# Optimization experiments

Hardware: AMD Instinct MI355X
Metric: run time of the kernel (lower is better)

The kernel has to match this reference:

```python
import jax, jax.numpy as jnp
import numpy as np

B, S, D, H = 2, 2048, 1024, 16
DK = D // H

def setup_inputs() -> dict:
    key = jax.random.key(0)
    ks = jax.random.split(key, 8)
    q = jax.random.normal(ks[0], (B, S, D), dtype=jnp.float32)
    k = jax.random.normal(ks[1], (B, S, D), dtype=jnp.float32)
    v = jax.random.normal(ks[2], (B, S, D), dtype=jnp.float32)
    # causal mask [B, S, S]; masked_fill where mask == 0
    mask = jnp.broadcast_to(jnp.tril(jnp.ones((S, S), dtype=jnp.int32)), (B, S, S))
    sc = 1.0 / np.sqrt(D)
    w_q = jax.random.normal(ks[3], (D, D), dtype=jnp.float32) * sc
    w_k = jax.random.normal(ks[4], (D, D), dtype=jnp.float32) * sc
    w_v = jax.random.normal(ks[5], (D, D), dtype=jnp.float32) * sc
    w_o = jax.random.normal(ks[6], (D, D), dtype=jnp.float32) * sc
    b_o = jnp.zeros((D,), dtype=jnp.float32)
    return {"query": q, "key": k, "value": v, "mask": mask,
            "w_q": w_q, "w_k": w_k, "w_v": w_v, "w_o": w_o, "b_o": b_o}

def reference(query, key, value, mask, w_q, w_k, w_v, w_o, b_o):
    # torch nn.Linear: y = x @ W.T
    def split_heads(x):
        return x.reshape(B, S, H, DK).transpose(0, 2, 1, 3)  # [B,H,S,DK]
    Q = split_heads(query @ w_q.T)
    K = split_heads(key @ w_k.T)
    V = split_heads(value @ w_v.T)
    scores = jnp.einsum('bhsd,bhtd->bhst', Q, K) / np.sqrt(DK)  # [B,H,S,S]
    m = mask[:, None, :, :]  # broadcast over heads
    scores = jnp.where(m == 0, jnp.float32(-1e9), scores)
    attn = jax.nn.softmax(scores, axis=-1)
    # dropout is identity in eval mode
    out = jnp.einsum('bhst,bhtd->bhsd', attn, V)  # [B,H,S,DK]
    out = out.transpose(0, 2, 1, 3).reshape(B, S, D)
    out = out @ w_o.T + b_o
    return (out, attn)
```

## Files before the change

kernel.cpp:

```cpp
#include <hip/hip_runtime.h>
#include <hip/hip_bf16.h>

#define S_LEN 2048
#define DMODEL 1024
#define NHEAD 16
#define DKH 64
#define NBATCH 2
#define NBH (NBATCH * NHEAD)
#define MROWS (NBATCH * S_LEN)
#define C1 0.18033688011112042f
#define C2 28.853900817779268f

typedef short bf16x8 __attribute__((ext_vector_type(8)));
typedef float f32x16 __attribute__((ext_vector_type(16)));
typedef float f32x4 __attribute__((ext_vector_type(4)));

typedef __attribute__((address_space(3))) void lds_void;
typedef __attribute__((address_space(1))) const void gbl_void;

__device__ __forceinline__ ushort f2bf(float f) {
  __hip_bfloat16 h = __float2bfloat16(f);
  union { __hip_bfloat16 h; ushort u; } c; c.h = h; return c.u;
}

__device__ __forceinline__ uint pack2(float a, float b) {
  float2 t; t.x = a; t.y = b;
  __hip_bfloat162 h = __float22bfloat162_rn(t);
  union { __hip_bfloat162 h; uint u; } c; c.h = h; return c.u;
}

__device__ __forceinline__ float bf2f(ushort u) {
  union { float f; uint u; } c; c.u = ((uint)u) << 16; return c.f;
}

__device__ __forceinline__ void gld16(void* lds, const void* g) {
  __builtin_amdgcn_global_load_lds((gbl_void*)(uintptr_t)g,
                                   (lds_void*)(uintptr_t)lds, 16, 0, 0);
}

__device__ __forceinline__ void gload_tile128(char* lds, const ushort* src, int strideE,
                                              int wid, int lane) {
#pragma unroll
  for (int j = 0; j < 4; j++) {
    int r = wid * 32 + j * 8 + (lane >> 3);
    int c = lane & 7;
    const char* g = (const char*)(src + (size_t)r * strideE) + ((c ^ (r & 7)) << 4);
    gld16(lds + wid * 4096 + j * 1024, g);
  }
}

__device__ __forceinline__ bf16x8 lds_frag(const char* base, int row, int kbyte) {
  int byte = row * 128 + kbyte;
  byte ^= (row & 7) << 4;
  return *(const bf16x8*)(base + byte);
}

__device__ __forceinline__ void tile_load_regs(const ushort* src, int srcStride,
                                               int tid, uint4& a, uint4& b) {
  int r = tid >> 2, cb = (tid & 3) * 32;
  const char* s = (const char*)(src + (size_t)r * srcStride) + cb;
  a = *(const uint4*)s;
  b = *(const uint4*)(s + 16);
}

__device__ __forceinline__ void tile_write_lds(char* dst, int tid,
                                               const uint4& a, const uint4& b) {
  int r = tid >> 2, cb = (tid & 3) * 32;
  int base = r * 128 + cb;
  int sw = (r & 7) << 4;
  *(uint4*)(dst + (base ^ sw)) = a;
  *(uint4*)(dst + ((base + 16) ^ sw)) = b;
}

__global__ __launch_bounds__(256) void cvt_kernel(
    const float* __restrict__ s0, ushort* __restrict__ d0,
    const float* __restrict__ s1, ushort* __restrict__ d1,
    const float* __restrict__ s2, ushort* __restrict__ d2,
    const float* __restrict__ s3, ushort* __restrict__ d3,
    const float* __restrict__ s4, ushort* __restrict__ d4,
    const float* __restrict__ s5, ushort* __restrict__ d5,
    const float* __restrict__ s6, ushort* __restrict__ d6) {
  const float* src; ushort* dst; int n;
  switch (blockIdx.y) {
    case 0: src = s0; dst = d0; n = MROWS * DMODEL; break;
    case 1: src = s1; dst = d1; n = MROWS * DMODEL; break;
    case 2: src = s2; dst = d2; n = MROWS * DMODEL; break;
    case 3: src = s3; dst = d3; n = DMODEL * DMODEL; break;
    case 4: src = s4; dst = d4; n = DMODEL * DMODEL; break;
    case 5: src = s5; dst = d5; n = DMODEL * DMODEL; break;
    default: src = s6; dst = d6; n = DMODEL * DMODEL; break;
  }
  for (size_t i = ((size_t)blockIdx.x * 256 + threadIdx.x) * 8; i < (size_t)n;
       i += (size_t)gridDim.x * 256 * 8) {
    float4 a = *(const float4*)(src + i);
    float4 b = *(const float4*)(src + i + 4);
    uint4 o = { pack2(a.x, a.y), pack2(a.z, a.w), pack2(b.x, b.y), pack2(b.z, b.w) };
    *(uint4*)(dst + i) = o;
  }
}

__global__ __launch_bounds__(256) void proj_kernel(
    const ushort* __restrict__ Xq, const ushort* __restrict__ Wq, ushort* __restrict__ Oq,
    const ushort* __restrict__ Xk, const ushort* __restrict__ Wk, ushort* __restrict__ Ok,
    const ushort* __restrict__ Xv, const ushort* __restrict__ Wv, ushort* __restrict__ Ov) {
  __shared__ char smem[34816];
  char* Xt = smem;
  char* Wt = smem + 16384;
  const ushort* X; const ushort* W; ushort* outH;
  if (blockIdx.z == 0)      { X = Xq; W = Wq; outH = Oq; }
  else if (blockIdx.z == 1) { X = Xk; W = Wk; outH = Ok; }
  else                      { X = Xv; W = Wv; outH = Ov; }

  int bm = blockIdx.x, bn = blockIdx.y;
  int tid = threadIdx.x;
  int lane = tid & 63, wid = tid >> 6;
  int l31 = lane & 31, hi = lane >> 5;
  int wr = wid >> 1, wc = wid & 1;
  f32x16 acc[2][2] = {};

  for (int kt = 0; kt < 1024; kt += 64) {
    __syncthreads();
    gload_tile128(Xt, X + (size_t)bm * 128 * 1024 + kt, 1024, wid, lane);
    gload_tile128(Wt, W + (size_t)bn * 128 * 1024 + kt, 1024, wid, lane);
    __syncthreads();
#pragma unroll
    for (int kk = 0; kk < 4; kk++) {
      bf16x8 a0 = lds_frag(Xt, 64 * wr + l31,      kk * 32 + hi * 16);
      bf16x8 a1 = lds_frag(Xt, 64 * wr + 32 + l31, kk * 32 + hi * 16);
      bf16x8 b0 = lds_frag(Wt, 64 * wc + l31,      kk * 32 + hi * 16);
      bf16x8 b1 = lds_frag(Wt, 64 * wc + 32 + l31, kk * 32 + hi * 16);
      acc[0][0] = __builtin_amdgcn_mfma_f32_32x32x16_bf16(a0, b0, acc[0][0], 0, 0, 0);
      acc[0][1] = __builtin_amdgcn_mfma_f32_32x32x16_bf16(a0, b1, acc[0][1], 0, 0, 0);
      acc[1][0] = __builtin_amdgcn_mfma_f32_32x32x16_bf16(a1, b0, acc[1][0], 0, 0, 0);
      acc[1][1] = __builtin_amdgcn_mfma_f32_32x32x16_bf16(a1, b1, acc[1][1], 0, 0, 0);
    }
  }
  __syncthreads();
  if (blockIdx.z != 2) {
    ushort (*ot)[136] = (ushort (*)[136])smem;
#pragma unroll
    for (int mi = 0; mi < 2; mi++)
#pragma unroll
      for (int ni = 0; ni < 2; ni++) {
        int col = wc * 64 + ni * 32 + l31;
#pragma unroll
        for (int rr = 0; rr < 16; rr++) {
          int row = wr * 64 + mi * 32 + (rr & 3) + 8 * (rr >> 2) + 4 * hi;
          ot[row][col] = f2bf(acc[mi][ni][rr]);
        }
      }
    __syncthreads();
    int r2 = tid >> 1, half = tid & 1;
    int m = bm * 128 + r2, b = m >> 11, s = m & 2047;
    int h = bn * 2 + half;
    ushort* dst = outH + ((size_t)(b * NHEAD + h) * S_LEN + s) * DKH;
    const ushort* srow = &ot[r2][half * 64];
#pragma unroll
    for (int j = 0; j < 8; j++)
      *(uint4*)(dst + j * 8) = *(const uint4*)(srow + j * 8);
  } else {
    ushort (*otT)[136] = (ushort (*)[136])smem;
#pragma unroll
    for (int mi = 0; mi < 2; mi++)
#pragma unroll
      for (int ni = 0; ni < 2; ni++) {
        int col = wc * 64 + ni * 32 + l31;
#pragma unroll
        for (int rr = 0; rr < 16; rr++) {
          int row = wr * 64 + mi * 32 + (rr & 3) + 8 * (rr >> 2) + 4 * hi;
          otT[col][row] = f2bf(acc[mi][ni][rr]);
        }
      }
    __syncthreads();
    int col2 = tid >> 1, sh = (tid & 1) * 64;
    int b = bm >> 4, s0 = (bm & 15) * 128;
    int h = bn * 2 + (col2 >> 6), d = col2 & 63;
    ushort* dst = outH + ((size_t)(b * NHEAD + h) * DKH + d) * S_LEN + s0 + sh;
    const ushort* srow = &otT[col2][sh];
#pragma unroll
    for (int j = 0; j < 8; j++)
      *(uint4*)(dst + j * 8) = *(const uint4*)(srow + j * 8);
  }
}

__global__ __launch_bounds__(256) void outproj_kernel(const ushort* __restrict__ A,
                                                      const ushort* __restrict__ W,
                                                      const float* __restrict__ bias,
                                                      float* __restrict__ out) {
  __shared__ char smem[33792];
  char* Xt = smem;
  char* Wt = smem + 16384;
  int bm = blockIdx.x, bn = blockIdx.y;
  int tid = threadIdx.x;
  int lane = tid & 63, wid = tid >> 6;
  int l31 = lane & 31, hi = lane >> 5;
  int wr = wid >> 1, wc = wid & 1;
  f32x16 acc[2][2] = {};

  for (int kt = 0; kt < 1024; kt += 64) {
    __syncthreads();
    gload_tile128(Xt, A + (size_t)bm * 128 * 1024 + kt, 1024, wid, lane);
    gload_tile128(Wt, W + (size_t)bn * 128 * 1024 + kt, 1024, wid, lane);
    __syncthreads();
#pragma unroll
    for (int kk = 0; kk < 4; kk++) {
      bf16x8 a0 = lds_frag(Xt, 64 * wr + l31,      kk * 32 + hi * 16);
      bf16x8 a1 = lds_frag(Xt, 64 * wr + 32 + l31, kk * 32 + hi * 16);
      bf16x8 b0 = lds_frag(Wt, 64 * wc + l31,      kk * 32 + hi * 16);
      bf16x8 b1 = lds_frag(Wt, 64 * wc + 32 + l31, kk * 32 + hi * 16);
      acc[0][0] = __builtin_amdgcn_mfma_f32_32x32x16_bf16(a0, b0, acc[0][0], 0, 0, 0);
      acc[0][1] = __builtin_amdgcn_mfma_f32_32x32x16_bf16(a0, b1, acc[0][1], 0, 0, 0);
      acc[1][0] = __builtin_amdgcn_mfma_f32_32x32x16_bf16(a1, b0, acc[1][0], 0, 0, 0);
      acc[1][1] = __builtin_amdgcn_mfma_f32_32x32x16_bf16(a1, b1, acc[1][1], 0, 0, 0);
    }
  }
  for (int mi = 0; mi < 2; mi++) {
    __syncthreads();
    {
      float (*of)[132] = (float (*)[132])smem;
#pragma unroll
      for (int ni = 0; ni < 2; ni++) {
        int col = wc * 64 + ni * 32 + l31;
        float bv = bias[bn * 128 + col];
#pragma unroll
        for (int rr = 0; rr < 16; rr++) {
          int lrow = wr * 32 + (rr & 3) + 8 * (rr >> 2) + 4 * hi;
          of[lrow][col] = acc[mi][ni][rr] + bv;
        }
      }
    }
    __syncthreads();
    {
      float (*of)[132] = (float (*)[132])smem;
      int lr = tid >> 2, ck = (tid & 3) * 32;
      int m = bm * 128 + (lr >> 5) * 64 + mi * 32 + (lr & 31);
      float* dst = out + (size_t)m * DMODEL + bn * 128 + ck;
#pragma unroll
      for (int j = 0; j < 8; j++)
        *(float4*)(dst + j * 4) = *(const float4*)(&of[lr][ck] + j * 4);
    }
  }
}

__global__ __launch_bounds__(256) void attn_kernel(const ushort* __restrict__ Qh,
                                                   const ushort* __restrict__ Kh,
                                                   const ushort* __restrict__ VTh,
                                                   float* __restrict__ attn,
                                                   ushort* __restrict__ Oc) {
  __shared__ char smem[58112];
  char* Kt0 = smem;
  char* Kt1 = smem + 8192;
  char* Vtb = smem + 16384;
  char* Pt0 = smem + 40960;
  char* Pt1 = smem + 49152;
  float* lpart = (float*)(smem + 57344);
  float* lfin  = lpart + 128;

  int bid = blockIdx.x;
  int xcd = bid & 7, idx = bid >> 3;
  int bh = (idx & 3) * 8 + xcd;
  int qx = idx >> 2;

  int tid = threadIdx.x;
  int wid = tid >> 6, lane = tid & 63;
  int l31 = lane & 31, hi = lane >> 5;
  int wr = wid >> 1, wc = wid & 1;

  const ushort* Kbase = Kh  + (size_t)bh * S_LEN * DKH;
  const ushort* Vbase = VTh + (size_t)bh * DKH * S_LEN;

  for (int half = 0; half < 2; half++) {
    int qb = half ? (31 - qx) : qx;
    int nt = qb + 1;
    int qg = qb * 64 + 32 * wc + l31;

    __syncthreads();

    bf16x8 qf[4];
    {
      const ushort* qrow = Qh + ((size_t)bh * S_LEN + qb * 64 + 32 * wc + l31) * DKH + hi * 8;
#pragma unroll
      for (int kk = 0; kk < 4; kk++) qf[kk] = *(const bf16x8*)(qrow + kk * 16);
    }

    {
      int zstart = nt * 64;
      f32x4 z4 = {0.f, 0.f, 0.f, 0.f};
      for (int rg = 0; rg < 4; rg++) {
        float* dst = attn + ((size_t)bh * S_LEN + qb * 64 + (tid >> 4) + rg * 16) * S_LEN;
        for (int c = zstart + (tid & 15) * 4; c < S_LEN; c += 64)
          __builtin_nontemporal_store(z4, (f32x4*)(dst + c));
      }
    }

    {
      uint4 a, b;
      tile_load_regs(Kbase, DKH, tid, a, b);
      tile_write_lds(Kt0, tid, a, b);
    }
    __syncthreads();
    float l_ln = 0.f;
    for (int kb = 0; kb < nt; kb++) {
      char* cur = (kb & 1) ? Kt1 : Kt0;
      char* nxt = (kb & 1) ? Kt0 : Kt1;
      uint4 pa, pb;
      bool pre = (kb + 1 < nt);
      if (pre) tile_load_regs(Kbase + (size_t)(kb + 1) * 64 * DKH, DKH, tid, pa, pb);
      f32x16 sacc = {};
      __builtin_amdgcn_s_setprio(1);
#pragma unroll
      for (int kk = 0; kk < 4; kk++) {
        bf16x8 a = lds_frag(cur, 32 * wr + l31, kk * 32 + hi * 16);
        sacc = __builtin_amdgcn_mfma_f32_32x32x16_bf16(a, qf[kk], sacc, 0, 0, 0);
      }
      __builtin_amdgcn_s_setprio(0);
      int kbase_g = kb * 64 + 32 * wr + 4 * hi;
      if (kb == qb) {
#pragma unroll
        for (int rr = 0; rr < 16; rr++) {
          int kg = kbase_g + (rr & 3) + 8 * (rr >> 2);
          float fs = fminf(fmaf(sacc[rr], C1, -C2), 86.f);
          l_ln += (kg > qg) ? 0.f : exp2f(fs);
        }
      } else {
#pragma unroll
        for (int rr = 0; rr < 16; rr++)
          l_ln += exp2f(fminf(fmaf(sacc[rr], C1, -C2), 86.f));
      }
      if (pre) tile_write_lds(nxt, tid, pa, pb);
      __syncthreads();
    }
    {
      float L = l_ln + __shfl_xor(l_ln, 32);
      if (lane < 32) lpart[wid * 32 + l31] = L;
    }
    __syncthreads();
    if (tid < 64) {
      int wcq = tid >> 5, qq = tid & 31;
      lfin[tid] = 1.0f / (lpart[wcq * 32 + qq] + lpart[(wcq + 2) * 32 + qq]);
    }
    __syncthreads();
    float liq = lfin[32 * wc + l31];

    f32x16 oacc = {};
    {
      uint4 ka, kb2, va, vb2;
      tile_load_regs(Kbase, DKH, tid, ka, kb2);
      tile_load_regs(Vbase, S_LEN, tid, va, vb2);
      tile_write_lds(Kt0, tid, ka, kb2);
      tile_write_lds(Vtb, tid, va, vb2);
    }
    int vcur_i = 0;
    __syncthreads();
    for (int kb = 0; kb < nt; kb++) {
      char* kcur = (kb & 1) ? Kt1 : Kt0;
      char* knxt = (kb & 1) ? Kt0 : Kt1;
      char* pcur = (kb & 1) ? Pt1 : Pt0;
      char* vcur = Vtb + vcur_i * 8192;
      int vnxt_i = (vcur_i == 2) ? 0 : vcur_i + 1;
      char* vnxt = Vtb + vnxt_i * 8192;
      uint4 ka, kb2, va, vb2;
      bool pre = (kb + 1 < nt);
      if (pre) {
        tile_load_regs(Kbase + (size_t)(kb + 1) * 64 * DKH, DKH, tid, ka, kb2);
        tile_load_regs(Vbase + (size_t)(kb + 1) * 64, S_LEN, tid, va, vb2);
      }
      f32x16 sacc = {};
      __builtin_amdgcn_s_setprio(1);
#pragma unroll
      for (int kk = 0; kk < 4; kk++) {
        bf16x8 a = lds_frag(kcur, 32 * wr + l31, kk * 32 + hi * 16);
        sacc = __builtin_amdgcn_mfma_f32_32x32x16_bf16(a, qf[kk], sacc, 0, 0, 0);
      }
      __builtin_amdgcn_s_setprio(0);
      int kbase_g = kb * 64 + 32 * wr + 4 * hi;
      float pv[16];
      if (kb == qb) {
#pragma unroll
        for (int rr = 0; rr < 16; rr++) {
          int kg = kbase_g + (rr & 3) + 8 * (rr >> 2);
          float fs = fminf(fmaf(sacc[rr], C1, -C2), 86.f);
          pv[rr] = (kg > qg) ? 0.f : exp2f(fs) * liq;
        }
      } else {
#pragma unroll
        for (int rr = 0; rr < 16; rr++)
          pv[rr] = exp2f(fminf(fmaf(sacc[rr], C1, -C2), 86.f)) * liq;
      }
      {
        int row = 32 * wc + l31;
        int sw = (row & 7) << 4;
#pragma unroll
        for (int g = 0; g < 4; g++) {
          uint2 pb2 = { pack2(pv[4 * g], pv[4 * g + 1]), pack2(pv[4 * g + 2], pv[4 * g + 3]) };
          int byte = row * 128 + (32 * wr + 8 * g + 4 * hi) * 2;
          *(uint2*)(pcur + (byte ^ sw)) = pb2;
        }
      }
      if (pre) {
        tile_write_lds(knxt, tid, ka, kb2);
        tile_write_lds(vnxt, tid, va, vb2);
      }
      __syncthreads();
      __builtin_amdgcn_s_setprio(1);
#pragma unroll
      for (int kk = 0; kk < 4; kk++) {
        bf16x8 a = lds_frag(pcur, 32 * wr + l31, kk * 32 + hi * 16);
        bf16x8 b = lds_frag(vcur, 32 * wc + l31, kk * 32 + hi * 16);
        oacc = __builtin_amdgcn_mfma_f32_32x32x16_bf16(a, b, oacc, 0, 0, 0);
      }
      __builtin_amdgcn_s_setprio(0);
      {
        const float* abase = attn + ((size_t)bh * S_LEN + qb * 64) * S_LEN + kb * 64;
#pragma unroll
        for (int r = 0; r < 4; r++) {
          int row = r * 16 + (tid >> 4);
          int colf = (tid & 15) * 4;
          int byte = (row * 128 + colf * 2) ^ ((row & 7) << 4);
          ushort4 u = *(const ushort4*)(pcur + byte);
          f32x4 f = { bf2f(u.x), bf2f(u.y), bf2f(u.z), bf2f(u.w) };
          __builtin_nontemporal_store(f, (f32x4*)((float*)abase + (size_t)row * S_LEN + colf));
        }
      }
      vcur_i = vnxt_i;
    }

    __syncthreads();
    float* Os = (float*)smem;
    {
      int col = 32 * wc + l31;
#pragma unroll
      for (int rr = 0; rr < 16; rr++) {
        int row = 32 * wr + (rr & 3) + 8 * (rr >> 2) + 4 * hi;
        Os[row * 64 + col] = oacc[rr];
      }
    }
    __syncthreads();
    {
      int b = bh >> 4, h = bh & 15;
      int r = tid >> 2, c0 = (tid & 3) * 16;
      uint w[8];
#pragma unroll
      for (int j = 0; j < 8; j++)
        w[j] = pack2(Os[r * 64 + c0 + 2 * j], Os[r * 64 + c0 + 2 * j + 1]);
      ushort* dst = Oc + ((size_t)(b * S_LEN + qb * 64 + r)) * DMODEL + h * 64 + c0;
      *(uint4*)dst = *(uint4*)&w[0];
      *(uint4*)(dst + 8) = *(uint4*)&w[4];
    }
  }
}

extern "C" void kernel_launch(void* const* d_in, const int* in_sizes, int n_in,
                              void* d_out, int out_size, void* d_ws, size_t ws_size,
                              hipStream_t stream) {
  (void)in_sizes; (void)n_in; (void)out_size; (void)ws_size;
  const float* q  = (const float*)d_in[0];
  const float* k  = (const float*)d_in[1];
  const float* v  = (const float*)d_in[2];
  const float* wq = (const float*)d_in[4];
  const float* wk = (const float*)d_in[5];
  const float* wv = (const float*)d_in[6];
  const float* wo = (const float*)d_in[7];
  const float* bo = (const float*)d_in[8];

  float* out  = (float*)d_out;
  float* attn = out + (size_t)MROWS * DMODEL;

  char* ws = (char*)d_ws;
  const size_t XSZ = (size_t)MROWS * DMODEL * sizeof(ushort);
  const size_t WSZ = (size_t)DMODEL * DMODEL * sizeof(ushort);
  ushort* Xq  = (ushort*)(ws);
  ushort* Xk  = (ushort*)(ws + XSZ);
  ushort* Xv  = (ushort*)(ws + 2 * XSZ);
  ushort* Wqb = (ushort*)(ws + 3 * XSZ);
  ushort* Wkb = (ushort*)(ws + 3 * XSZ + WSZ);
  ushort* Wvb = (ushort*)(ws + 3 * XSZ + 2 * WSZ);
  ushort* Wob = (ushort*)(ws + 3 * XSZ + 3 * WSZ);
  char*   ws2 = ws + 3 * XSZ + 4 * WSZ;
  ushort* Qh  = (ushort*)(ws2);
  ushort* Kh  = (ushort*)(ws2 + XSZ);
  ushort* VTh = (ushort*)(ws2 + 2 * XSZ);
  ushort* Oc  = (ushort*)(ws2 + 3 * XSZ);

  dim3 blk(256);
  hipLaunchKernelGGL(cvt_kernel, dim3(512, 7), blk, 0, stream,
                     q, Xq, k, Xk, v, Xv, wq, Wqb, wk, Wkb, wv, Wvb, wo, Wob);
  hipLaunchKernelGGL(proj_kernel, dim3(32, 8, 3), blk, 0, stream,
                     Xq, Wqb, Qh, Xk, Wkb, Kh, Xv, Wvb, VTh);
  hipLaunchKernelGGL(attn_kernel, dim3(512), blk, 0, stream, Qh, Kh, VTh, attn, Oc);
  hipLaunchKernelGGL(outproj_kernel, dim3(32, 8), blk, 0, stream, Oc, Wob, bo, out);
}
```

Baseline: 204.6 us.

## Merge row-sum passes of both query blocks into one shared K sweep

The softmax-denominator pass for the small and large query blocks now shares a single loop over K tiles, so each K tile is loaded into LDS once and used by both blocks' MFMAs. The separate first pass for the small block, with its own K reloads and barriers, goes away. Q fragments for both halves are kept in registers for the whole kernel, which raises register pressure and may cost occupancy.

After: 210.8 us. 1.03x slower.

```diff
diff --git a/kernel.cpp b/kernel.cpp
--- a/kernel.cpp
+++ b/kernel.cpp
@@ -247,14 +247,16 @@
                                                    const ushort* __restrict__ VTh,
                                                    float* __restrict__ attn,
                                                    ushort* __restrict__ Oc) {
-  __shared__ char smem[58112];
+  __shared__ char smem[58880];
   char* Kt0 = smem;
   char* Kt1 = smem + 8192;
   char* Vtb = smem + 16384;
   char* Pt0 = smem + 40960;
   char* Pt1 = smem + 49152;
-  float* lpart = (float*)(smem + 57344);
-  float* lfin  = lpart + 128;
+  float* lpartS = (float*)(smem + 57344);
+  float* lpartL = lpartS + 128;
+  float* lfinS  = lpartL + 128;
+  float* lfinL  = lfinS + 64;
 
   int bid = blockIdx.x;
   int xcd = bid & 7, idx = bid >> 3;
@@ -269,78 +271,106 @@
   const ushort* Kbase = Kh  + (size_t)bh * S_LEN * DKH;
   const ushort* Vbase = VTh + (size_t)bh * DKH * S_LEN;
 
+  int qbA[2] = { qx, 31 - qx };
+  int ntS = qx + 1, ntL = 32 - qx;
+
+  bf16x8 qf[2][4];
+#pragma unroll
+  for (int h = 0; h < 2; h++) {
+    const ushort* qrow = Qh + ((size_t)bh * S_LEN + qbA[h] * 64 + 32 * wc + l31) * DKH + hi * 8;
+#pragma unroll
+    for (int kk = 0; kk < 4; kk++) qf[h][kk] = *(const bf16x8*)(qrow + kk * 16);
+  }
+
+#pragma unroll
+  for (int h = 0; h < 2; h++) {
+    int zstart = (qbA[h] + 1) * 64;
+    f32x4 z4 = {0.f, 0.f, 0.f, 0.f};
+    for (int rg = 0; rg < 4; rg++) {
+      float* dst = attn + ((size_t)bh * S_LEN + qbA[h] * 64 + (tid >> 4) + rg * 16) * S_LEN;
+      for (int c = zstart + (tid & 15) * 4; c < S_LEN; c += 64)
+        __builtin_nontemporal_store(z4, (f32x4*)(dst + c));
+    }
+  }
+
+  {
+    uint4 a, b;
+    tile_load_regs(Kbase, DKH, tid, a, b);
+    tile_write_lds(Kt0, tid, a, b);
+  }
+  __syncthreads();
+  float lS = 0.f, lL = 0.f;
+  int qgS = qbA[0] * 64 + 32 * wc + l31;
+  for (int kb = 0; kb < ntL; kb++) {
+    char* cur = (kb & 1) ? Kt1 : Kt0;
+    char* nxt = (kb & 1) ? Kt0 : Kt1;
+    uint4 pa, pb;
+    bool pre = (kb + 1 < ntL);
+    if (pre) tile_load_regs(Kbase + (size_t)(kb + 1) * 64 * DKH, DKH, tid, pa, pb);
+    bool small = (kb < ntS);
+    f32x16 saccL = {}, saccS = {};
+    __builtin_amdgcn_s_setprio(1);
+#pragma unroll
+    for (int kk = 0; kk < 4; kk++) {
+      bf16x8 a = lds_frag(cur, 32 * wr + l31, kk * 32 + hi * 16);
+      saccL = __builtin_amdgcn_mfma_f32_32x32x16_bf16(a, qf[1][kk], saccL, 0, 0, 0);
+      if (small)
+        saccS = __builtin_amdgcn_mfma_f32_32x32x16_bf16(a, qf[0][kk], saccS, 0, 0, 0);
+    }
+    __builtin_amdgcn_s_setprio(0);
+    int kbase_g = kb * 64 + 32 * wr + 4 * hi;
+    if (kb == qbA[1]) {
+      int qgL = qbA[1] * 64 + 32 * wc + l31;
+#pragma unroll
+      for (int rr = 0; rr < 16; rr++) {
+        int kg = kbase_g + (rr & 3) + 8 * (rr >> 2);
+        float fs = fminf(fmaf(saccL[rr], C1, -C2), 86.f);
+        lL += (kg > qgL) ? 0.f : exp2f(fs);
+      }
+    } else {
+#pragma unroll
+      for (int rr = 0; rr < 16; rr++)
+        lL += exp2f(fminf(fmaf(saccL[rr], C1, -C2), 86.f));
+    }
+    if (small) {
+      if (kb == qbA[0]) {
+#pragma unroll
+        for (int rr = 0; rr < 16; rr++) {
+          int kg = kbase_g + (rr & 3) + 8 * (rr >> 2);
+          float fs = fminf(fmaf(saccS[rr], C1, -C2), 86.f);
+          lS += (kg > qgS) ? 0.f : exp2f(fs);
+        }
+      } else {
+#pragma unroll
+        for (int rr = 0; rr < 16; rr++)
+          lS += exp2f(fminf(fmaf(saccS[rr], C1, -C2), 86.f));
+      }
+    }
+    if (pre) tile_write_lds(nxt, tid, pa, pb);
+    __syncthreads();
+  }
+  {
+    float LS = lS + __shfl_xor(lS, 32);
+    float LL = lL + __shfl_xor(lL, 32);
+    if (lane < 32) { lpartS[wid * 32 + l31] = LS; lpartL[wid * 32 + l31] = LL; }
+  }
+  __syncthreads();
+  if (tid < 64) {
+    int wcq = tid >> 5, qq = tid & 31;
+    lfinS[tid] = 1.0f / (lpartS[wcq * 32 + qq] + lpartS[(wcq + 2) * 32 + qq]);
+    lfinL[tid] = 1.0f / (lpartL[wcq * 32 + qq] + lpartL[(wcq + 2) * 32 + qq]);
+  }
+  __syncthreads();
+  float liqA[2] = { lfinS[32 * wc + l31], lfinL[32 * wc + l31] };
+
+#pragma unroll
   for (int half = 0; half < 2; half++) {
-    int qb = half ? (31 - qx) : qx;
+    int qb = qbA[half];
     int nt = qb + 1;
     int qg = qb * 64 + 32 * wc + l31;
-
-    __syncthreads();
-
-    bf16x8 qf[4];
-    {
-      const ushort* qrow = Qh + ((size_t)bh * S_LEN + qb * 64 + 32 * wc + l31) * DKH + hi * 8;
-#pragma unroll
-      for (int kk = 0; kk < 4; kk++) qf[kk] = *(const bf16x8*)(qrow + kk * 16);
-    }
-
-    {
-      int zstart = nt * 64;
-      f32x4 z4 = {0.f, 0.f, 0.f, 0.f};
-      for (int rg = 0; rg < 4; rg++) {
-        float* dst = attn + ((size_t)bh * S_LEN + qb * 64 + (tid >> 4) + rg * 16) * S_LEN;
-        for (int c = zstart + (tid & 15) * 4; c < S_LEN; c += 64)
-          __builtin_nontemporal_store(z4, (f32x4*)(dst + c));
-      }
-    }
-
-    {
-      uint4 a, b;
-      tile_load_regs(Kbase, DKH, tid, a, b);
-      tile_write_lds(Kt0, tid, a, b);
-    }
-    __syncthreads();
-    float l_ln = 0.f;
-    for (int kb = 0; kb < nt; kb++) {
-      char* cur = (kb & 1) ? Kt1 : Kt0;
-      char* nxt = (kb & 1) ? Kt0 : Kt1;
-      uint4 pa, pb;
-      bool pre = (kb + 1 < nt);
-      if (pre) tile_load_regs(Kbase + (size_t)(kb + 1) * 64 * DKH, DKH, tid, pa, pb);
-      f32x16 sacc = {};
-      __builtin_amdgcn_s_setprio(1);
-#pragma unroll
-      for (int kk = 0; kk < 4; kk++) {
-        bf16x8 a = lds_frag(cur, 32 * wr + l31, kk * 32 + hi * 16);
-        sacc = __builtin_amdgcn_mfma_f32_32x32x16_bf16(a, qf[kk], sacc, 0, 0, 0);
-      }
-      __builtin_amdgcn_s_setprio(0);
-      int kbase_g = kb * 64 + 32 * wr + 4 * hi;
-      if (kb == qb) {
-#pragma unroll
-        for (int rr = 0; rr < 16; rr++) {
-          int kg = kbase_g + (rr & 3) + 8 * (rr >> 2);
-          float fs = fminf(fmaf(sacc[rr], C1, -C2), 86.f);
-          l_ln += (kg > qg) ? 0.f : exp2f(fs);
-        }
-      } else {
-#pragma unroll
-        for (int rr = 0; rr < 16; rr++)
-          l_ln += exp2f(fminf(fmaf(sacc[rr], C1, -C2), 86.f));
-      }
-      if (pre) tile_write_lds(nxt, tid, pa, pb);
-      __syncthreads();
-    }
-    {
-      float L = l_ln + __shfl_xor(l_ln, 32);
-      if (lane < 32) lpart[wid * 32 + l31] = L;
-    }
-    __syncthreads();
-    if (tid < 64) {
-      int wcq = tid >> 5, qq = tid & 31;
-      lfin[tid] = 1.0f / (lpart[wcq * 32 + qq] + lpart[(wcq + 2) * 32 + qq]);
-    }
-    __syncthreads();
-    float liq = lfin[32 * wc + l31];
+    float liq = liqA[half];
+
+    __syncthreads();
 
     f32x16 oacc = {};
     {
@@ -370,7 +400,7 @@
 #pragma unroll
       for (int kk = 0; kk < 4; kk++) {
         bf16x8 a = lds_frag(kcur, 32 * wr + l31, kk * 32 + hi * 16);
-        sacc = __builtin_amdgcn_mfma_f32_32x32x16_bf16(a, qf[kk], sacc, 0, 0, 0);
+        sacc = __builtin_amdgcn_mfma_f32_32x32x16_bf16(a, qf[half][kk], sacc, 0, 0, 0);
       }
       __builtin_amdgcn_s_setprio(0);
       int kbase_g = kb * 64 + 32 * wr + 4 * hi;
```
